# Kernel optimization log

Hardware: AMD Instinct MI355X
Metric: run time of the kernel (lower is better)

Reference implementation:

```python
import jax, jax.numpy as jnp
from jax import lax
import numpy as np

EPS = 1e-7          # BCE clamp
SMOOTH = 1.0        # Dice smoothing
INT_INF = jnp.int32(2**31 - 1)


def _bce_dice(p, t):
    """BCE + Dice loss (standard BCEDiceLoss): p, t float32 in [0,1]."""
    pc = jnp.clip(p, EPS, 1.0 - EPS)
    bce = -jnp.mean(t * jnp.log(pc) + (1.0 - t) * jnp.log1p(-pc))
    inter = jnp.sum(p * t)
    dice = 1.0 - (2.0 * inter + SMOOTH) / (jnp.sum(p) + jnp.sum(t) + SMOOTH)
    return bce + dice


def _ccl(mask):
    """4-connected component labeling per batch image.
    mask: [B,H,W] bool. Returns (labels, init_labels) int32; 0 = background.
    Iterative min-label propagation to a fixpoint (lax.while_loop)."""
    B, H, W = mask.shape
    init = jnp.where(mask, jnp.arange(1, B * H * W + 1, dtype=jnp.int32).reshape(B, H, W), 0)

    def step(lab):
        big = jnp.where(mask, lab, INT_INF)
        pad_h = jnp.full((B, 1, W), INT_INF, jnp.int32)
        pad_w = jnp.full((B, H, 1), INT_INF, jnp.int32)
        up    = jnp.concatenate([big[:, 1:, :], pad_h], axis=1)
        down  = jnp.concatenate([pad_h, big[:, :-1, :]], axis=1)
        left  = jnp.concatenate([big[:, :, 1:], pad_w], axis=2)
        right = jnp.concatenate([pad_w, big[:, :, :-1]], axis=2)
        m = jnp.minimum(big, jnp.minimum(jnp.minimum(up, down), jnp.minimum(left, right)))
        return jnp.where(mask, m, 0)

    def cond(c):
        return c[1]

    def body(c):
        new = step(c[0])
        return (new, jnp.any(new != c[0]))

    lab, _ = lax.while_loop(cond, body, (init, jnp.array(True)))
    return lab, init


def _forward(pred_out, target_mask, num_target_classes):
    f32 = jnp.float32
    B, C, H, W = pred_out.shape
    pred_masks = jnp.argmax(pred_out, axis=1)      # [B,H,W] int
    tm = target_mask[:, 0]                         # [B,H,W] int

    # background-vs-background BCEDice term
    res = _bce_dice((pred_masks == 0).astype(f32), (tm == 0).astype(f32))

    ph = jnp.zeros((B, H, W), f32)    # pred_placeholder
    pho = jnp.zeros((B, H, W), f32)   # pred_placeholder_out
    last_i = jnp.int32(1)

    # fixed loop over predicted classes (torch loops over unique values;
    # here: loop 1..C-1 gated by presence so absent classes are no-ops)
    for v in range(1, C):
        cur = pred_masks == v                       # class-v mask
        present = jnp.any(cur)
        lab, init = _ccl(cur)
        # number of connected components = pixels that kept their seed label
        n_comp = jnp.sum((lab == init) & cur).astype(jnp.int32)
        has_bg = jnp.any(~cur).astype(jnp.int32)    # 0 in cur_uniq?
        # sum_c (c_mask + last_i) over components == cur + n_comp*last_i everywhere
        inc = cur.astype(f32) + (n_comp * last_i).astype(f32)
        ph = jnp.where(present, ph + inc, ph)
        pho = jnp.where(cur, pred_out[:, v], pho)
        last_i = last_i + jnp.where(present, n_comp + has_bg, 0)

    # loop over nonzero target ids (bounded by num_target_classes), gated by presence
    for t in range(1, num_target_classes):
        target_m = tm == t
        present = jnp.any(target_m)
        n = jnp.sum(target_m)
        # torch.median(ph[target_m]): lower median of masked values
        vals = jnp.where(target_m.reshape(-1), ph.reshape(-1), jnp.inf)
        med = jnp.sort(vals)[jnp.maximum((n - 1) // 2, 0)]
        tm_f = target_m.astype(f32)
        contrib = _bce_dice(pho * (ph == med).astype(f32), tm_f)
        extra = jnp.sum(pho * ((ph != med) & target_m).astype(f32)) / jnp.maximum(n, 1).astype(f32)
        res = res + jnp.where(present, contrib + extra, 0.0)

    # len(torch.unique(target_mask)) with values in [0, num_target_classes)
    n_unique = jnp.sum(jnp.stack([jnp.any(tm == t) for t in range(num_target_classes)]).astype(jnp.int32))
    return res / (2 * n_unique + 1).astype(f32)


def setup_inputs() -> dict:
    key = jax.random.key(0)
    k1, k2 = jax.random.split(key)
    B, C, H, W = 8, 5, 768, 768
    pred_out = jax.random.uniform(k1, (B, C, H, W), dtype=jnp.float32)
    target_mask = jax.random.randint(k2, (B, 1, H, W), 0, 4, dtype=jnp.int32)
    return {"pred_out": pred_out, "target_mask": target_mask, "num_target_classes": 4}


def reference(pred_out, target_mask, num_target_classes):
    return _forward(pred_out, target_mask, num_target_classes)
```

## Files before the change

### kernel.cpp

```cpp
#include <hip/hip_runtime.h>
#include <stdint.h>
#include <math.h>

#define B_ 8
#define C_ 5
#define H_ 768
#define W_ 768
#define HW_ (H_*W_)
#define HWq (HW_/4)
#define NPIX (B_*HW_)
#define TB 8
#define INVAL 0xFFFFFFFFu
#define LN2F 0.69314718056f
#define BIASF 16.2f
#define TILE 64
#define TPR 12
#define TPC 12
#define NTILES (B_*TPR*TPC)
#define NNODES (NTILES*256)
#define SEAMS_PER_IMG (11*768)
#define NB_HALF (B_*SEAMS_PER_IMG)
#define NB_TOT (2*NB_HALF)
#define SEAMBLK (NB_TOT/256)
#define NCOPY 16

typedef unsigned long long ull;

static __device__ __forceinline__ unsigned pload(const unsigned* P, unsigned i) {
  return __hip_atomic_load(&P[i], __ATOMIC_RELAXED, __HIP_MEMORY_SCOPE_AGENT);
}
static __device__ unsigned findRootG(unsigned* P, unsigned i) {
  unsigned p = pload(P, i);
  if (p == i) return i;
  unsigned gp = pload(P, p);
  while (p != gp) {
    __hip_atomic_store(&P[i], gp, __ATOMIC_RELAXED, __HIP_MEMORY_SCOPE_AGENT);
    i = p; p = gp; gp = pload(P, p);
  }
  return p;
}
static __device__ bool uniteG(unsigned* P, unsigned a, unsigned b) {
  a = findRootG(P, a);
  b = findRootG(P, b);
  while (a != b) {
    if (a < b) { unsigned t = a; a = b; b = t; }
    unsigned old = atomicCAS(&P[a], a, b);
    if (old == a) return true;
    a = findRootG(P, old);
    b = findRootG(P, b);
  }
  return false;
}
static __device__ __forceinline__ unsigned ploadL(const unsigned* P, unsigned i) {
  return __hip_atomic_load(&P[i], __ATOMIC_RELAXED, __HIP_MEMORY_SCOPE_WORKGROUP);
}
static __device__ unsigned findRootL(const unsigned* P, unsigned i) {
  unsigned p = ploadL(P, i) & 0xFFFFu;
  while (p != i) { i = p; p = ploadL(P, i) & 0xFFFFu; }
  return i;
}
static __device__ void uniteL(unsigned* P, unsigned a, unsigned b) {
  a = findRootL(P, a);
  b = findRootL(P, b);
  while (a != b) {
    if (a < b) { unsigned t = a; a = b; b = t; }
    unsigned old = atomicCAS(&P[a], 0xFFFF0000u | a, 0xFFFF0000u | b);
    if (old == (0xFFFF0000u | a)) return;
    a = findRootL(P, old & 0xFFFFu);
    b = findRootL(P, b);
  }
}

__global__ __launch_bounds__(512, 8) void k_stats_ccl(
    const float* __restrict__ pred, const int* __restrict__ tgt,
    unsigned short* __restrict__ border, unsigned* __restrict__ P2,
    unsigned* __restrict__ rootcnt, double* __restrict__ sp)
{
  __shared__ ull h[NCOPY][41];
  __shared__ unsigned lab[TILE*TILE];
  __shared__ unsigned lclsw[TILE*TILE/4];
  __shared__ unsigned s_rt[4];
  unsigned char* lcls = (unsigned char*)lclsw;

  for (int i = threadIdx.x; i < NCOPY*41; i += 512) (&h[0][0])[i] = 0ull;
  if (threadIdx.x < 4) s_rt[threadIdx.x] = 0u;
  if (threadIdx.x < 256) {
    unsigned n = (unsigned)blockIdx.x * 256u + threadIdx.x;
    P2[n] = n;
  }
  __syncthreads();

  const int cp = threadIdx.x & (NCOPY - 1);
  int blk = blockIdx.x;
  int b = blk / (TPR*TPC);
  int rem = blk - b * (TPR*TPC);
  int ty0 = (rem / TPR) * TILE;
  int tx0 = (rem - (rem / TPR) * TPR) * TILE;

  {
    const int baseq = ty0 * (W_/4) + (tx0 >> 2);
    const float4* pp0 = (const float4*)pred + (size_t)b * (C_*HWq) + baseq;
    const int4*   tp0 = (const int4*)tgt   + (size_t)b * HWq        + baseq;
#pragma unroll
    for (int qq = 0; qq < 2; ++qq) {
      const int q = threadIdx.x + qq * 512;
      const int qrow = q >> 4, qcol = q & 15;
      const int o = qrow * (W_/4) + qcol;
      float4 a0 = pp0[o];
      float4 a1 = pp0[o + HWq];
      float4 a2 = pp0[o + 2*HWq];
      float4 a3 = pp0[o + 3*HWq];
      float4 a4 = pp0[o + 4*HWq];
      int4 t4 = tp0[o];
      unsigned pk = 0u;
#pragma unroll
      for (int j = 0; j < 4; ++j) {
        float v0 = ((const float*)&a0)[j];
        float v1 = ((const float*)&a1)[j];
        float v2 = ((const float*)&a2)[j];
        float v3 = ((const float*)&a3)[j];
        float v4 = ((const float*)&a4)[j];
        int tt = ((const int*)&t4)[j];
        float best = v0; int bc = 0;
        if (v1 > best) { best = v1; bc = 1; }
        if (v2 > best) { best = v2; bc = 2; }
        if (v3 > best) { best = v3; bc = 3; }
        if (v4 > best) { best = v4; bc = 4; }
        unsigned tu = (unsigned)tt; if (tu >= TB) tu = TB - 1;
        ull w;
        if (bc) {
          float pc = fminf(fmaxf(best, 1e-7f), 1.0f - 1e-7f);
          float l2p = __log2f(pc);
          float l2m = __log2f(1.0f - pc);
          float logit = (l2p - l2m) * LN2F;
          float mag   = -l2m * LN2F;
          w = (1ull << 57)
            | ((ull)__float2uint_rn(best * 4096.0f) << 38)
            | ((ull)__float2uint_rn((logit + BIASF) * 64.0f) << 20)
            | (ull)__float2uint_rn(mag * 64.0f);
        } else {
          w = 1ull << 57;
        }
        atomicAdd(&h[cp][(int)tu * C_ + bc], w);
        pk |= ((unsigned)bc) << (8 * j);
      }
      lclsw[q] = pk;
    }
  }
  __syncthreads();

  const int r = threadIdx.x >> 3, sub = threadIdx.x & 7;
  const int seg = r * 64 + sub * 8;
  union { uint2 d2; unsigned char bch[8]; unsigned w[2]; } A, D;
  A.d2 = *(const uint2*)&lclsw[r * 16 + sub * 2];
  if (r < 63) D.d2 = *(const uint2*)&lclsw[(r + 1) * 16 + sub * 2];
  else D.d2 = make_uint2(0, 0);
  unsigned rb = (sub < 7) ? (unsigned)lcls[seg + 8] : 0u;
#pragma unroll
  for (int m = 0; m < 2; ++m) {
    uint4 lw;
    unsigned* lp = (unsigned*)&lw;
#pragma unroll
    for (int k = 0; k < 4; ++k) {
      int li = seg + m * 4 + k;
      unsigned c = (A.w[m] >> (8 * k)) & 255u;
      lp[k] = c ? (0xFFFF0000u | (unsigned)li) : INVAL;
    }
    *(uint4*)&lab[seg + m * 4] = lw;
  }
  __syncthreads();

#pragma unroll
  for (int j = 0; j < 8; ++j) {
    unsigned c = A.bch[j];
    if (!c) continue;
    int li = seg + j;
    unsigned cr = (j < 7) ? (unsigned)A.bch[j + 1] : rb;
    if (cr == c) uniteL(lab, li, li + 1);
    if (D.bch[j] == c) uniteL(lab, li, li + 64);
  }
  __syncthreads();

#pragma unroll
  for (int m = 0; m < 2; ++m) {
    uint4 lw = *(const uint4*)&lab[seg + m * 4];
    const unsigned* lp = (const unsigned*)&lw;
#pragma unroll
    for (int k = 0; k < 4; ++k) {
      int li = seg + m * 4 + k;
      unsigned c = A.bch[m * 4 + k];
      if (c && (lp[k] & 0xFFFFu) == (unsigned)li) atomicAdd(&s_rt[c - 1], 1u);
    }
  }
  unsigned bc_c = 0, bc_rt = 0;
  if (threadIdx.x < 256) {
    int bp = threadIdx.x;
    int tx, ty;
    if (bp < 64)       { ty = 0;  tx = bp; }
    else if (bp < 128) { ty = 63; tx = bp - 64; }
    else if (bp < 192) { tx = 0;  ty = bp - 128; }
    else               { tx = 63; ty = bp - 192; }
    int li = ty * 64 + tx;
    bc_c = lcls[li];
    if (bc_c) {
      bc_rt = findRootL(lab, (unsigned)li);
      atomicMin(&lab[bc_rt], ((unsigned)bp << 16) | bc_rt);
    }
  }
  __syncthreads();
  if (threadIdx.x < 256) {
    unsigned sub2 = bc_c ? (lab[bc_rt] >> 16) : 0u;
    border[blk * 256 + threadIdx.x] = (unsigned short)((bc_c << 8) | sub2);
  }
  if (threadIdx.x < 4) rootcnt[blk * 4 + threadIdx.x] = s_rt[threadIdx.x];
  if (threadIdx.x < 160) {
    int slot = threadIdx.x >> 2, comp = threadIdx.x & 3;
    double s = 0.0;
#pragma unroll
    for (int cc = 0; cc < NCOPY; ++cc) {
      ull w = h[cc][slot];
      if (comp == 0)      s += (double)(w >> 57);
      else if (comp == 1) s += (double)((w >> 38) & 0x7FFFFull) * (1.0/4096.0);
      else if (comp == 2) s += (double)((w >> 20) & 0x3FFFFull) * (1.0/64.0);
      else                s += (double)(w & 0x1FFFFull) * (1.0/64.0);
    }
    sp[(size_t)blk * 160 + threadIdx.x] = s;
  }
}

__global__ __launch_bounds__(256) void k_seam(const unsigned short* __restrict__ border,
                                              unsigned* __restrict__ P2,
                                              unsigned* __restrict__ smcnt,
                                              const double* __restrict__ sp,
                                              double* __restrict__ spf)
{
  __shared__ unsigned s_sub[4];
  __shared__ double red[256];
  if (threadIdx.x < 4) s_sub[threadIdx.x] = 0u;
  __syncthreads();
  int idx = blockIdx.x * blockDim.x + threadIdx.x;
  if (idx < NB_TOT) {
    int tA, tB, pA, pB;
    if (idx < NB_HALF) {
      int b = idx / SEAMS_PER_IMG;
      int r = idx - b * SEAMS_PER_IMG;
      int seam = r / W_;
      int x = r - seam * W_;
      int tj = x >> 6, k = x & 63;
      tA = (b * TPC + seam) * TPR + tj;
      tB = tA + TPR;
      pA = tA * 256 + 64 + k;
      pB = tB * 256 + 0 + k;
    } else {
      int i2 = idx - NB_HALF;
      int b = i2 / SEAMS_PER_IMG;
      int r = i2 - b * SEAMS_PER_IMG;
      int seam = r / H_;
      int y = r - seam * H_;
      int ti = y >> 6, k = y & 63;
      tA = (b * TPC + ti) * TPR + seam;
      tB = tA + 1;
      pA = tA * 256 + 192 + k;
      pB = tB * 256 + 128 + k;
    }
    unsigned a16 = border[pA];
    unsigned b16 = border[pB];
    unsigned ca = a16 >> 8, cb = b16 >> 8;
    if (ca && ca == cb) {
      if (uniteG(P2, (unsigned)tA * 256u + (a16 & 255u),
                     (unsigned)tB * 256u + (b16 & 255u)))
        atomicAdd(&s_sub[ca - 1], 1u);
    }
  }
  __syncthreads();
  if (threadIdx.x < 4) smcnt[blockIdx.x * 4 + threadIdx.x] = s_sub[threadIdx.x];
  if (blockIdx.x < 160) {
    double s = 0.0;
    for (int j = threadIdx.x; j < NTILES; j += 256) s += sp[(size_t)j * 160 + blockIdx.x];
    red[threadIdx.x] = s;
    __syncthreads();
    for (int off = 128; off; off >>= 1) {
      if (threadIdx.x < off) red[threadIdx.x] += red[threadIdx.x + off];
      __syncthreads();
    }
    if (threadIdx.x == 0) spf[blockIdx.x] = red[0];
  }
}

#define SH_CNT(t,c)   shist[((t)*C_+(c))*4 + 0]
#define SH_PRED(t,c)  shist[((t)*C_+(c))*4 + 1]
#define SH_LRAW(t,c)  shist[((t)*C_+(c))*4 + 2]
#define SH_MAG(t,c)   shist[((t)*C_+(c))*4 + 3]
__global__ __launch_bounds__(256) void k_final(
    const double* __restrict__ spf, const unsigned* __restrict__ rootcnt,
    const unsigned* __restrict__ smcnt, const int* __restrict__ ntcp,
    float* __restrict__ out)
{
  __shared__ double shist[160];
  __shared__ double s_col[C_][3];
  __shared__ unsigned s_cnti[TB*C_];
  __shared__ unsigned s_ctot[C_];
  __shared__ unsigned s_nc[4], s_sm[4];
  __shared__ float s_ph[C_];
  __shared__ double s_term[TB];
  __shared__ int s_NT;
  __shared__ int s_nun;

  if (threadIdx.x < 4) { s_nc[threadIdx.x] = 0u; s_sm[threadIdx.x] = 0u; }
  if (threadIdx.x < TB) s_term[threadIdx.x] = 0.0;
  __syncthreads();
  if (threadIdx.x < 160) shist[threadIdx.x] = spf[threadIdx.x];
  {
    unsigned a = 0;
    for (int j = threadIdx.x; j < NTILES * 4; j += 256) a += rootcnt[j];
    if (a) atomicAdd(&s_nc[threadIdx.x & 3], a);
  }
  {
    unsigned a = 0;
    for (int j = threadIdx.x; j < SEAMBLK * 4; j += 256) a += smcnt[j];
    if (a) atomicAdd(&s_sm[threadIdx.x & 3], a);
  }
  if (threadIdx.x == 0) {
    int NT = ntcp[0];
    if (NT < 1) NT = 1;
    if (NT > TB) NT = TB;
    s_NT = NT;
  }
  __syncthreads();

  if (threadIdx.x < TB * C_) s_cnti[threadIdx.x] = (unsigned)llrint(shist[threadIdx.x * 4]);
  __syncthreads();

  if (threadIdx.x < C_) {
    int c = threadIdx.x;
    double sc = 0.0, sp2 = 0.0, sl = 0.0;
    unsigned ct = 0;
#pragma unroll
    for (int t = 0; t < TB; ++t) {
      sc += SH_CNT(t, c);
      sp2 += SH_PRED(t, c);
      sl += -SH_MAG(t, c);
      ct += s_cnti[t * C_ + c];
    }
    s_col[c][0] = sc; s_col[c][1] = sp2; s_col[c][2] = sl;
    s_ctot[c] = ct;
  }
  __syncthreads();

  if (threadIdx.x == 0) {
#pragma unroll
    for (int cc = 0; cc < C_; ++cc) {
      float ph = 0.0f;
      int li = 1;
#pragma unroll
      for (int v = 1; v < C_; ++v) {
        unsigned ncv = s_nc[v - 1] - s_sm[v - 1];
        if (s_ctot[v] > 0) {
          int prod = (int)(ncv * (unsigned)li);
          float sv = (float)prod;
          float inc = ((cc == v) ? 1.0f : 0.0f) + sv;
          ph = ph + inc;
          li = li + (int)ncv + ((s_ctot[v] < (unsigned)NPIX) ? 1 : 0);
        }
      }
      s_ph[cc] = ph;
    }
  }
  __syncthreads();

  const float EPSF = 1e-7f;
  const double L1 = (double)logf(1.0f - EPSF);
  const double M1 = (double)log1pf(-(1.0f - EPSF));
  const double L0 = (double)logf(EPSF);
  const double M0 = (double)log1pf(-EPSF);
  const double N = (double)NPIX;
  const double BIASD = (double)BIASF;
  const int NT = s_NT;

  if (threadIdx.x == 0) {
    double nt0 = 0;
#pragma unroll
    for (int c = 0; c < C_; ++c) nt0 += SH_CNT(0, c);
    double np1 = (double)s_ctot[0];
    double n11 = SH_CNT(0, 0);
    s_term[0] = -(n11*L1 + (nt0 - n11)*L0 + (np1 - n11)*M1 + (N - nt0 - np1 + n11)*M0) / N
                + 1.0 - (2.0*n11 + 1.0) / (np1 + nt0 + 1.0);
    int nun = 0;
    for (int t = 0; t < NT; ++t) {
      long long s = 0;
#pragma unroll
      for (int c = 0; c < C_; ++c) s += (long long)s_cnti[t * C_ + c];
      if (s) nun++;
    }
    s_nun = nun;
  } else if (threadIdx.x < (unsigned)NT) {
    int t = threadIdx.x;
    long long ntti = 0;
#pragma unroll
    for (int c = 0; c < C_; ++c) ntti += (long long)s_cnti[t * C_ + c];
    if (ntti != 0) {
      double ntt = 0;
#pragma unroll
      for (int c = 0; c < C_; ++c) ntt += SH_CNT(t, c);
      float ph0 = s_ph[0], ph1 = s_ph[1], ph2 = s_ph[2], ph3 = s_ph[3], ph4 = s_ph[4];
      float pht[C_] = {ph0, ph1, ph2, ph3, ph4};
      int idx[C_] = {0, 1, 2, 3, 4};
#pragma unroll
      for (int i = 1; i < C_; ++i)
        for (int j = i; j > 0 && pht[idx[j]] < pht[idx[j-1]]; --j) {
          int tmp = idx[j]; idx[j] = idx[j-1]; idx[j-1] = tmp;
        }
      long long k = (ntti - 1) / 2;
      float med = pht[idx[C_ - 1]];
      long long cum = 0;
#pragma unroll
      for (int i = 0; i < C_; ++i) {
        cum += (long long)s_cnti[t * C_ + idx[i]];
        if (cum > k) { med = pht[idx[i]]; break; }
      }
      double A = 0, Bt = 0, inter = 0, sum_p = 0, ex = 0, nfg_t = 0, nfg_all = 0;
#pragma unroll
      for (int c = 1; c < C_; ++c) {
        double cnt_tc = SH_CNT(t, c);
        double mag_tc = SH_MAG(t, c);
        double spred_tc = SH_PRED(t, c);
        if (pht[c] == med) {
          double logit = SH_LRAW(t, c) - BIASD * cnt_tc;
          A += logit - mag_tc;
          inter += spred_tc;
          nfg_t += cnt_tc;
          nfg_all += s_col[c][0];
          sum_p += s_col[c][1];
          Bt += s_col[c][2] - (-mag_tc);
        } else {
          ex += spred_tc;
        }
      }
      double bce  = -(A + Bt + (ntt - nfg_t)*L0 + (N - ntt - (nfg_all - nfg_t))*M0) / N;
      double dice = 1.0 - (2.0*inter + 1.0) / (sum_p + ntt + 1.0);
      s_term[t] = bce + dice + ex / ntt;
    }
  }
  __syncthreads();
  if (threadIdx.x == 0) {
    double res = 0.0;
#pragma unroll
    for (int t = 0; t < TB; ++t) res += s_term[t];
    out[0] = (float)(res / (double)(2 * s_nun + 1));
  }
}

extern "C" void kernel_launch(void* const* d_in, const int* in_sizes, int n_in,
                              void* d_out, int out_size, void* d_ws, size_t ws_size,
                              hipStream_t stream) {
  const float* pred = (const float*)d_in[0];
  const int* tgt = (const int*)d_in[1];
  const int* ntc = (const int*)d_in[2];
  float* out = (float*)d_out;
  char* ws = (char*)d_ws;
  size_t off = 0;
  double* sp = (double*)(ws + off);              off += (size_t)NTILES * 160 * 8;
  double* spf = (double*)(ws + off);             off += 160 * 8;
  unsigned* P2 = (unsigned*)(ws + off);          off += (size_t)NNODES * 4;
  unsigned short* border = (unsigned short*)(ws + off); off += (size_t)NTILES * 256 * 2;
  unsigned* rootcnt = (unsigned*)(ws + off);     off += (size_t)NTILES * 4 * 4;
  unsigned* smcnt = (unsigned*)(ws + off);       off += (size_t)SEAMBLK * 4 * 4;

  hipLaunchKernelGGL(k_stats_ccl, dim3(NTILES), dim3(512), 0, stream,
                     pred, tgt, border, P2, rootcnt, sp);
  hipLaunchKernelGGL(k_seam, dim3(SEAMBLK), dim3(256), 0, stream,
                     border, P2, smcnt, sp, spf);
  hipLaunchKernelGGL(k_final, dim3(1), dim3(256), 0, stream,
                     spf, rootcnt, smcnt, ntc, out);
}
```

Measured before the change: 183.9 us.

## Shrink CCL tiles from 64x64 to 32x32 with 256-thread blocks

```diff
diff --git a/kernel.cpp b/kernel.cpp
--- a/kernel.cpp
+++ b/kernel.cpp
@@ -13,12 +13,13 @@
 #define INVAL 0xFFFFFFFFu
 #define LN2F 0.69314718056f
 #define BIASF 16.2f
-#define TILE 64
-#define TPR 12
-#define TPC 12
+#define TILE 32
+#define TPR 24
+#define TPC 24
 #define NTILES (B_*TPR*TPC)
-#define NNODES (NTILES*256)
-#define SEAMS_PER_IMG (11*768)
+#define NPT 128
+#define NNODES (NTILES*NPT)
+#define SEAMS_PER_IMG (23*768)
 #define NB_HALF (B_*SEAMS_PER_IMG)
 #define NB_TOT (2*NB_HALF)
 #define SEAMBLK (NB_TOT/256)
@@ -71,7 +72,7 @@
   }
 }
 
-__global__ __launch_bounds__(512, 8) void k_stats_ccl(
+__global__ __launch_bounds__(256, 8) void k_stats_ccl(
     const float* __restrict__ pred, const int* __restrict__ tgt,
     unsigned short* __restrict__ border, unsigned* __restrict__ P2,
     unsigned* __restrict__ rootcnt, double* __restrict__ sp)
@@ -82,10 +83,10 @@
   __shared__ unsigned s_rt[4];
   unsigned char* lcls = (unsigned char*)lclsw;
 
-  for (int i = threadIdx.x; i < NCOPY*41; i += 512) (&h[0][0])[i] = 0ull;
+  for (int i = threadIdx.x; i < NCOPY*41; i += 256) (&h[0][0])[i] = 0ull;
   if (threadIdx.x < 4) s_rt[threadIdx.x] = 0u;
-  if (threadIdx.x < 256) {
-    unsigned n = (unsigned)blockIdx.x * 256u + threadIdx.x;
+  if (threadIdx.x < NPT) {
+    unsigned n = (unsigned)blockIdx.x * NPT + threadIdx.x;
     P2[n] = n;
   }
   __syncthreads();
@@ -94,123 +95,114 @@
   int blk = blockIdx.x;
   int b = blk / (TPR*TPC);
   int rem = blk - b * (TPR*TPC);
-  int ty0 = (rem / TPR) * TILE;
-  int tx0 = (rem - (rem / TPR) * TPR) * TILE;
-
+  int trow = rem / TPR;
+  int ty0 = trow * TILE;
+  int tx0 = (rem - trow * TPR) * TILE;
+
+  unsigned pk = 0u;
   {
     const int baseq = ty0 * (W_/4) + (tx0 >> 2);
-    const float4* pp0 = (const float4*)pred + (size_t)b * (C_*HWq) + baseq;
-    const int4*   tp0 = (const int4*)tgt   + (size_t)b * HWq        + baseq;
-#pragma unroll
-    for (int qq = 0; qq < 2; ++qq) {
-      const int q = threadIdx.x + qq * 512;
-      const int qrow = q >> 4, qcol = q & 15;
-      const int o = qrow * (W_/4) + qcol;
-      float4 a0 = pp0[o];
-      float4 a1 = pp0[o + HWq];
-      float4 a2 = pp0[o + 2*HWq];
-      float4 a3 = pp0[o + 3*HWq];
-      float4 a4 = pp0[o + 4*HWq];
-      int4 t4 = tp0[o];
-      unsigned pk = 0u;
-#pragma unroll
-      for (int j = 0; j < 4; ++j) {
-        float v0 = ((const float*)&a0)[j];
-        float v1 = ((const float*)&a1)[j];
-        float v2 = ((const float*)&a2)[j];
-        float v3 = ((const float*)&a3)[j];
-        float v4 = ((const float*)&a4)[j];
-        int tt = ((const int*)&t4)[j];
-        float best = v0; int bc = 0;
-        if (v1 > best) { best = v1; bc = 1; }
-        if (v2 > best) { best = v2; bc = 2; }
-        if (v3 > best) { best = v3; bc = 3; }
-        if (v4 > best) { best = v4; bc = 4; }
-        unsigned tu = (unsigned)tt; if (tu >= TB) tu = TB - 1;
-        ull w;
-        if (bc) {
-          float pc = fminf(fmaxf(best, 1e-7f), 1.0f - 1e-7f);
-          float l2p = __log2f(pc);
-          float l2m = __log2f(1.0f - pc);
-          float logit = (l2p - l2m) * LN2F;
-          float mag   = -l2m * LN2F;
-          w = (1ull << 57)
-            | ((ull)__float2uint_rn(best * 4096.0f) << 38)
-            | ((ull)__float2uint_rn((logit + BIASF) * 64.0f) << 20)
-            | (ull)__float2uint_rn(mag * 64.0f);
-        } else {
-          w = 1ull << 57;
-        }
-        atomicAdd(&h[cp][(int)tu * C_ + bc], w);
-        pk |= ((unsigned)bc) << (8 * j);
+    const int qrow = threadIdx.x >> 3, qcol = threadIdx.x & 7;
+    const int o = qrow * (W_/4) + qcol;
+    const float4* pp = (const float4*)pred + (size_t)b * (C_*HWq) + baseq + o;
+    float4 a0 = pp[0];
+    float4 a1 = pp[HWq];
+    float4 a2 = pp[2*HWq];
+    float4 a3 = pp[3*HWq];
+    float4 a4 = pp[4*HWq];
+    int4 t4 = ((const int4*)tgt)[(size_t)b * HWq + baseq + o];
+#pragma unroll
+    for (int j = 0; j < 4; ++j) {
+      float v0 = ((const float*)&a0)[j];
+      float v1 = ((const float*)&a1)[j];
+      float v2 = ((const float*)&a2)[j];
+      float v3 = ((const float*)&a3)[j];
+      float v4 = ((const float*)&a4)[j];
+      int tt = ((const int*)&t4)[j];
+      float best = v0; int bc = 0;
+      if (v1 > best) { best = v1; bc = 1; }
+      if (v2 > best) { best = v2; bc = 2; }
+      if (v3 > best) { best = v3; bc = 3; }
+      if (v4 > best) { best = v4; bc = 4; }
+      unsigned tu = (unsigned)tt; if (tu >= TB) tu = TB - 1;
+      ull w;
+      if (bc) {
+        float pc = fminf(fmaxf(best, 1e-7f), 1.0f - 1e-7f);
+        float l2p = __log2f(pc);
+        float l2m = __log2f(1.0f - pc);
+        float logit = (l2p - l2m) * LN2F;
+        float mag   = -l2m * LN2F;
+        w = (1ull << 57)
+          | ((ull)__float2uint_rn(best * 4096.0f) << 38)
+          | ((ull)__float2uint_rn((logit + BIASF) * 64.0f) << 20)
+          | (ull)__float2uint_rn(mag * 64.0f);
+      } else {
+        w = 1ull << 57;
       }
-      lclsw[q] = pk;
-    }
+      atomicAdd(&h[cp][(int)tu * C_ + bc], w);
+      pk |= ((unsigned)bc) << (8 * j);
+    }
+    lclsw[threadIdx.x] = pk;
   }
   __syncthreads();
 
   const int r = threadIdx.x >> 3, sub = threadIdx.x & 7;
-  const int seg = r * 64 + sub * 8;
-  union { uint2 d2; unsigned char bch[8]; unsigned w[2]; } A, D;
-  A.d2 = *(const uint2*)&lclsw[r * 16 + sub * 2];
-  if (r < 63) D.d2 = *(const uint2*)&lclsw[(r + 1) * 16 + sub * 2];
-  else D.d2 = make_uint2(0, 0);
-  unsigned rb = (sub < 7) ? (unsigned)lcls[seg + 8] : 0u;
-#pragma unroll
-  for (int m = 0; m < 2; ++m) {
+  const int seg = r * TILE + sub * 4;
+  unsigned Dw = (r < TILE-1) ? lclsw[threadIdx.x + 8] : 0u;
+  unsigned rb = (sub < 7) ? (lclsw[threadIdx.x + 1] & 255u) : 0u;
+  {
     uint4 lw;
     unsigned* lp = (unsigned*)&lw;
 #pragma unroll
     for (int k = 0; k < 4; ++k) {
-      int li = seg + m * 4 + k;
-      unsigned c = (A.w[m] >> (8 * k)) & 255u;
+      int li = seg + k;
+      unsigned c = (pk >> (8 * k)) & 255u;
       lp[k] = c ? (0xFFFF0000u | (unsigned)li) : INVAL;
     }
-    *(uint4*)&lab[seg + m * 4] = lw;
-  }
-  __syncthreads();
-
-#pragma unroll
-  for (int j = 0; j < 8; ++j) {
-    unsigned c = A.bch[j];
+    *(uint4*)&lab[seg] = lw;
+  }
+  __syncthreads();
+
+#pragma unroll
+  for (int j = 0; j < 4; ++j) {
+    unsigned c = (pk >> (8 * j)) & 255u;
     if (!c) continue;
     int li = seg + j;
-    unsigned cr = (j < 7) ? (unsigned)A.bch[j + 1] : rb;
+    unsigned cr = (j < 3) ? ((pk >> (8 * (j + 1))) & 255u) : rb;
     if (cr == c) uniteL(lab, li, li + 1);
-    if (D.bch[j] == c) uniteL(lab, li, li + 64);
-  }
-  __syncthreads();
-
-#pragma unroll
-  for (int m = 0; m < 2; ++m) {
-    uint4 lw = *(const uint4*)&lab[seg + m * 4];
+    if (((Dw >> (8 * j)) & 255u) == c) uniteL(lab, li, li + TILE);
+  }
+  __syncthreads();
+
+  {
+    uint4 lw = *(const uint4*)&lab[seg];
     const unsigned* lp = (const unsigned*)&lw;
 #pragma unroll
     for (int k = 0; k < 4; ++k) {
-      int li = seg + m * 4 + k;
-      unsigned c = A.bch[m * 4 + k];
+      int li = seg + k;
+      unsigned c = (pk >> (8 * k)) & 255u;
       if (c && (lp[k] & 0xFFFFu) == (unsigned)li) atomicAdd(&s_rt[c - 1], 1u);
     }
   }
   unsigned bc_c = 0, bc_rt = 0;
-  if (threadIdx.x < 256) {
+  if (threadIdx.x < NPT) {
     int bp = threadIdx.x;
     int tx, ty;
-    if (bp < 64)       { ty = 0;  tx = bp; }
-    else if (bp < 128) { ty = 63; tx = bp - 64; }
-    else if (bp < 192) { tx = 0;  ty = bp - 128; }
-    else               { tx = 63; ty = bp - 192; }
-    int li = ty * 64 + tx;
+    if (bp < 32)       { ty = 0;       tx = bp; }
+    else if (bp < 64)  { ty = TILE-1;  tx = bp - 32; }
+    else if (bp < 96)  { tx = 0;       ty = bp - 64; }
+    else               { tx = TILE-1;  ty = bp - 96; }
+    int li = ty * TILE + tx;
     bc_c = lcls[li];
     if (bc_c) {
       bc_rt = findRootL(lab, (unsigned)li);
-      atomicMin(&lab[bc_rt], ((unsigned)bp << 16) | bc_rt);
-    }
-  }
-  __syncthreads();
-  if (threadIdx.x < 256) {
+      atomicMin(&lab[bc_rt], ((unsigned)threadIdx.x << 16) | bc_rt);
+    }
+  }
+  __syncthreads();
+  if (threadIdx.x < NPT) {
     unsigned sub2 = bc_c ? (lab[bc_rt] >> 16) : 0u;
-    border[blk * 256 + threadIdx.x] = (unsigned short)((bc_c << 8) | sub2);
+    border[blk * NPT + threadIdx.x] = (unsigned short)((bc_c << 8) | sub2);
   }
   if (threadIdx.x < 4) rootcnt[blk * 4 + threadIdx.x] = s_rt[threadIdx.x];
   if (threadIdx.x < 160) {
@@ -246,29 +238,29 @@
       int r = idx - b * SEAMS_PER_IMG;
       int seam = r / W_;
       int x = r - seam * W_;
-      int tj = x >> 6, k = x & 63;
+      int tj = x >> 5, k = x & 31;
       tA = (b * TPC + seam) * TPR + tj;
       tB = tA + TPR;
-      pA = tA * 256 + 64 + k;
-      pB = tB * 256 + 0 + k;
+      pA = tA * NPT + 32 + k;
+      pB = tB * NPT + 0 + k;
     } else {
       int i2 = idx - NB_HALF;
       int b = i2 / SEAMS_PER_IMG;
       int r = i2 - b * SEAMS_PER_IMG;
       int seam = r / H_;
       int y = r - seam * H_;
-      int ti = y >> 6, k = y & 63;
+      int ti = y >> 5, k = y & 31;
       tA = (b * TPC + ti) * TPR + seam;
       tB = tA + 1;
-      pA = tA * 256 + 192 + k;
-      pB = tB * 256 + 128 + k;
+      pA = tA * NPT + 96 + k;
+      pB = tB * NPT + 64 + k;
     }
     unsigned a16 = border[pA];
     unsigned b16 = border[pB];
     unsigned ca = a16 >> 8, cb = b16 >> 8;
     if (ca && ca == cb) {
-      if (uniteG(P2, (unsigned)tA * 256u + (a16 & 255u),
-                     (unsigned)tB * 256u + (b16 & 255u)))
+      if (uniteG(P2, (unsigned)tA * NPT + (a16 & 255u),
+                     (unsigned)tB * NPT + (b16 & 255u)))
         atomicAdd(&s_sub[ca - 1], 1u);
     }
   }
@@ -462,11 +454,11 @@
   double* sp = (double*)(ws + off);              off += (size_t)NTILES * 160 * 8;
   double* spf = (double*)(ws + off);             off += 160 * 8;
   unsigned* P2 = (unsigned*)(ws + off);          off += (size_t)NNODES * 4;
-  unsigned short* border = (unsigned short*)(ws + off); off += (size_t)NTILES * 256 * 2;
+  unsigned short* border = (unsigned short*)(ws + off); off += (size_t)NTILES * NPT * 2;
   unsigned* rootcnt = (unsigned*)(ws + off);     off += (size_t)NTILES * 4 * 4;
   unsigned* smcnt = (unsigned*)(ws + off);       off += (size_t)SEAMBLK * 4 * 4;
 
-  hipLaunchKernelGGL(k_stats_ccl, dim3(NTILES), dim3(512), 0, stream,
+  hipLaunchKernelGGL(k_stats_ccl, dim3(NTILES), dim3(256), 0, stream,
                      pred, tgt, border, P2, rootcnt, sp);
   hipLaunchKernelGGL(k_seam, dim3(SEAMBLK), dim3(256), 0, stream,
                      border, P2, smcnt, sp, spf);
```

After: 190.9 us. 1.04x slower.
